# Kernel optimization log

Measured on AMD Instinct MI355X. Metric: run time of the kernel, lower is better.

## Reference

```python
import jax, jax.numpy as jnp
from jax import lax
import numpy as np

B, C, H, W, HID = 16, 8, 512, 512, 16


def setup_inputs() -> dict:
    key = jax.random.key(0)
    k1, k2, k3, k4, k5 = jax.random.split(key, 5)
    x = jax.random.normal(k1, (B, C, H, W), dtype=jnp.float32)
    w1_w = jax.random.normal(k2, (HID, 4 * C), dtype=jnp.float32) * 0.1  # 1x1 conv 32->16
    w1_b = jax.random.normal(k3, (HID,), dtype=jnp.float32) * 0.1
    w2_w = jax.random.normal(k4, (C, HID), dtype=jnp.float32) * 0.1     # 1x1 conv 16->8, no bias
    update_mask = jax.random.randint(k5, (B, 1, H, W), 0, 2, dtype=jnp.int32)  # floor(rand+0.5)
    return {"x": x, "w1_w": w1_w, "w1_b": w1_b, "w2_w": w2_w, "update_mask": update_mask}


def _fixed_filters(dtype):
    ident = jnp.zeros((3, 3), dtype).at[1, 1].set(1.0)
    sobel_x = jnp.array([[-1.0, 0.0, 1.0], [-2.0, 0.0, 2.0], [-1.0, 0.0, 1.0]], dtype) / 8.0
    lap = jnp.array([[1.0, 2.0, 1.0], [2.0, -12.0, 2.0], [1.0, 2.0, 1.0]], dtype) / 16.0
    return jnp.stack([ident, sobel_x, sobel_x.T, lap])  # [4,3,3]


def _perception(x):
    b, c, h, w = x.shape
    filt = _fixed_filters(x.dtype)
    xp = jnp.pad(x, ((0, 0), (0, 0), (1, 1), (1, 1)), mode="wrap")  # circular pad
    y = lax.conv_general_dilated(
        xp.reshape(b * c, 1, h + 2, w + 2), filt[:, None], (1, 1), "VALID",
        dimension_numbers=("NCHW", "OIHW", "NCHW"))  # [b*c,4,h,w]
    return y.reshape(b, c * 4, h, w)  # channel-major: (c0f0..c0f3, c1f0.., ...)


def reference(x, w1_w, w1_b, w2_w, update_mask):
    dt = 1.0
    y = _perception(x)                                   # [B,4C,H,W]
    y = jax.nn.relu(jnp.einsum("bchw,oc->bohw", y, w1_w) + w1_b[None, :, None, None])
    y = jnp.einsum("bchw,oc->bohw", y, w2_w)             # [B,C,H,W]
    return x + dt * y * update_mask.astype(x.dtype)
```

## Files before the change

kernel.cpp:

```cpp
#include <hip/hip_runtime.h>
#include <stdint.h>


constexpr int B = 16, C = 8, H = 512, W = 512, HID = 16;
constexpr int HW = H * W;
constexpr int BUF = 3 * W;

#define PKFMA_S(acc, w, p) \
    asm("v_pk_fma_f32 %0, %1, %2, %0" : "+v"(acc) : "s"(w), "v"(p))
#define PKFMA_V(acc, a, b) \
    asm("v_pk_fma_f32 %0, %1, %2, %0" : "+v"(acc) : "v"(a), "v"(b))

typedef const __attribute__((address_space(1))) void* as1cp;
typedef __attribute__((address_space(3))) void* as3p;

__global__ void repack_weights(const float* __restrict__ w1w,
                               const float* __restrict__ w2w,
                               float2* __restrict__ wd) {
    const int i = blockIdx.x * 256 + threadIdx.x;
    if (i < 512) {
        const int c = i >> 6, r = i & 63, h = r >> 2, f = r & 3;
        const float v = w1w[h * 32 + c * 4 + f];
        wd[i] = make_float2(v, v);
    } else if (i < 640) {
        const float v = w2w[i - 512];
        wd[i] = make_float2(v, v);
    }
}

__global__ __launch_bounds__(256, 6) void nca_step_kernel(
    const float* __restrict__ x,
    const float* __restrict__ w1b,
    const int*   __restrict__ mask,
    float*       __restrict__ out,
    const float2* __restrict__ wd)
{
    __shared__ float S[2 * BUF];

    const int bid = blockIdx.x;
    const int l   = (bid & 7) * 1024 + (bid >> 3);
    const int b   = l >> 9;
    const int y   = l & (H - 1);

    const int tx   = threadIdx.x;
    const int x0   = tx << 1;
    const int lane = tx & 63;
    const int wv   = tx >> 6;

    const int ym = (y - 1) & (H - 1);
    const int yp = (y + 1) & (H - 1);
    const int xm1 = (x0 - 1) & (W - 1);
    const int xp2 = (x0 + 2) & (W - 1);

    const float* xb = x + (size_t)b * C * HW;
    const int pix = y * W + x0;

    const int hh = wv & 1;
    const int g1 = ((wv < 2) ? ym : y) * W + hh * 256 + lane * 4;
    const int l1 = ((wv < 2) ? 0 : W) + hh * 256;
    const int g2 = yp * W + hh * 256 + lane * 4;
    const int l2 = 2 * W + hh * 256;

#define STAGE(ch, bufo) do {                                               \
    const float* cb_ = xb + (ch) * HW;                                     \
    __builtin_amdgcn_global_load_lds((as1cp)(cb_ + g1),                    \
                                     (as3p)(S + (bufo) + l1), 16, 0, 0);   \
    if (wv < 2)                                                            \
        __builtin_amdgcn_global_load_lds((as1cp)(cb_ + g2),                \
                                         (as3p)(S + (bufo) + l2), 16, 0, 0); \
    } while (0)

#define COMPCH(ch, bufo) do {                                              \
    const float* R0 = S + (bufo);                                          \
    const float* R1 = R0 + W;                                              \
    const float* R2 = R1 + W;                                              \
    const float2 vm = *(const float2*)(R0 + x0);                           \
    const float2 vc = *(const float2*)(R1 + x0);                           \
    const float2 vp = *(const float2*)(R2 + x0);                           \
    const float cm[4] = {R0[xm1], vm.x, vm.y, R0[xp2]};                    \
    const float cc[4] = {R1[xm1], vc.x, vc.y, R1[xp2]};                    \
    const float cp[4] = {R2[xm1], vp.x, vp.y, R2[xp2]};                    \
    float s_[4], d_[4];                                                    \
    _Pragma("unroll") for (int i = 0; i < 4; ++i) {                        \
        s_[i] = fmaf(2.0f, cc[i], cm[i] + cp[i]);                          \
        d_[i] = cp[i] - cm[i]; }                                           \
    const float sx0  = (s_[2] - s_[0]) * 0.125f;                           \
    const float sx1  = (s_[3] - s_[1]) * 0.125f;                           \
    const float sy0  = fmaf(2.0f, d_[1], d_[0] + d_[2]) * 0.125f;          \
    const float sy1  = fmaf(2.0f, d_[2], d_[1] + d_[3]) * 0.125f;          \
    const float lap0 = fmaf(fmaf(2.0f, s_[1], s_[0] + s_[2]), 0.0625f, -cc[1]); \
    const float lap1 = fmaf(fmaf(2.0f, s_[2], s_[1] + s_[3]), 0.0625f, -cc[2]); \
    const float2 idn2 = make_float2(cc[1], cc[2]);                         \
    const float2 sx2  = make_float2(sx0, sx1);                             \
    const float2 sy2  = make_float2(sy0, sy1);                             \
    const float2 lp2  = make_float2(lap0, lap1);                           \
    const float2* wch = wd + (ch) * 64;                                    \
    _Pragma("unroll") for (int h = 0; h < HID; ++h) {                      \
        PKFMA_S(acc[h], wch[h * 4 + 0], idn2);                             \
        PKFMA_S(acc[h], wch[h * 4 + 1], sx2);                              \
        PKFMA_S(acc[h], wch[h * 4 + 2], sy2);                              \
        PKFMA_S(acc[h], wch[h * 4 + 3], lp2); } } while (0)

    const int2 m2 = *(const int2*)(mask + (size_t)b * HW + pix);

    float2 acc[HID];
#pragma unroll
    for (int h = 0; h < HID; ++h) {
        const float bv = w1b[h];
        acc[h] = make_float2(bv, bv);
    }

    STAGE(0, 0);
    __syncthreads();
    STAGE(1, BUF); COMPCH(0, 0);   __syncthreads();
    STAGE(2, 0);   COMPCH(1, BUF); __syncthreads();
    STAGE(3, BUF); COMPCH(2, 0);   __syncthreads();
    STAGE(4, 0);   COMPCH(3, BUF); __syncthreads();
    STAGE(5, BUF); COMPCH(4, 0);   __syncthreads();
    STAGE(6, 0);   COMPCH(5, BUF); __syncthreads();
    STAGE(7, BUF); COMPCH(6, 0);   __syncthreads();
                   COMPCH(7, BUF);

#undef STAGE
#undef COMPCH

#pragma unroll
    for (int h = 0; h < HID; ++h) {
        acc[h].x = fmaxf(acc[h].x, 0.0f);
        acc[h].y = fmaxf(acc[h].y, 0.0f);
    }

    const float2 mf = make_float2((float)m2.x, (float)m2.y);
    const float2* w2d = wd + 512;
    float* ob = out + (size_t)b * C * HW;

    float2 xo = *(const float2*)(xb + pix);
#pragma unroll
    for (int o = 0; o < C; ++o) {
        float2 xn;
        if (o + 1 < C) xn = *(const float2*)(xb + (o + 1) * HW + pix);
        float2 v = make_float2(0.0f, 0.0f);
#pragma unroll
        for (int h = 0; h < HID; ++h)
            PKFMA_S(v, w2d[o * 16 + h], acc[h]);
        PKFMA_V(xo, v, mf);
        *(float2*)(ob + o * HW + pix) = xo;
        xo = xn;
    }
}

extern "C" void kernel_launch(void* const* d_in, const int* in_sizes, int n_in,
                              void* d_out, int out_size, void* d_ws, size_t ws_size,
                              hipStream_t stream) {
    const float* x    = (const float*)d_in[0];
    const float* w1w  = (const float*)d_in[1];
    const float* w1b  = (const float*)d_in[2];
    const float* w2w  = (const float*)d_in[3];
    const int*   mask = (const int*)d_in[4];
    float* out = (float*)d_out;
    float2* wd = (float2*)d_ws;

    hipLaunchKernelGGL(repack_weights, dim3(3), dim3(256), 0, stream,
                       w1w, w2w, wd);
    hipLaunchKernelGGL(nca_step_kernel, dim3(B * H), dim3(256), 0, stream,
                       x, w1b, mask, out, wd);
}
```

Measured before the change: 96.07 us.

## Triple-buffer LDS staging with vmcnt waits and balanced per-wave row loads

Replaces the double-buffered channel staging with a three-deep LDS ring. Two channels are now in flight, and each stage waits only for its own loads via s_waitcnt vmcnt(2) before a raw s_barrier, instead of a full __syncthreads. Row loading is rebalanced so every wave issues two async global-to-LDS loads per stage. The fourth wave uses its slots to stage the mask row into LDS, and the mask is then read from LDS rather than with a separate global load. The aim is to hide global latency better in this memory-bound stencil. The cost is doubled LDS per block, which may limit occupancy, and the mask row being re-fetched redundantly on every stage.

```diff
diff --git a/kernel.cpp b/kernel.cpp
--- a/kernel.cpp
+++ b/kernel.cpp
@@ -4,12 +4,17 @@
 
 constexpr int B = 16, C = 8, H = 512, W = 512, HID = 16;
 constexpr int HW = H * W;
-constexpr int BUF = 3 * W;
+constexpr int BUF = 3 * W + 512;
 
 #define PKFMA_S(acc, w, p) \
     asm("v_pk_fma_f32 %0, %1, %2, %0" : "+v"(acc) : "s"(w), "v"(p))
 #define PKFMA_V(acc, a, b) \
     asm("v_pk_fma_f32 %0, %1, %2, %0" : "+v"(acc) : "v"(a), "v"(b))
+
+#define VMWAIT2 asm volatile("s_waitcnt vmcnt(2)" ::: "memory")
+#define VMWAIT0 asm volatile("s_waitcnt vmcnt(0)" ::: "memory")
+#define BARRIER do { __builtin_amdgcn_s_barrier(); \
+                     __builtin_amdgcn_sched_barrier(0); } while (0)
 
 typedef const __attribute__((address_space(1))) void* as1cp;
 typedef __attribute__((address_space(3))) void* as3p;
@@ -35,7 +40,7 @@
     float*       __restrict__ out,
     const float2* __restrict__ wd)
 {
-    __shared__ float S[2 * BUF];
+    __shared__ float S[3 * BUF];
 
     const int bid = blockIdx.x;
     const int l   = (bid & 7) * 1024 + (bid >> 3);
@@ -55,20 +60,24 @@
     const float* xb = x + (size_t)b * C * HW;
     const int pix = y * W + x0;
 
-    const int hh = wv & 1;
-    const int g1 = ((wv < 2) ? ym : y) * W + hh * 256 + lane * 4;
-    const int l1 = ((wv < 2) ? 0 : W) + hh * 256;
-    const int g2 = yp * W + hh * 256 + lane * 4;
-    const int l2 = 2 * W + hh * 256;
+    int r1f, l1, r2f, l2;
+    if (wv == 0)      { r1f = ym * W;       l1 = 0;       r2f = y * W;        l2 = W; }
+    else if (wv == 1) { r1f = ym * W + 256; l1 = 256;     r2f = y * W + 256;  l2 = W + 256; }
+    else if (wv == 2) { r1f = yp * W;       l1 = 2 * W;   r2f = yp * W + 256; l2 = 2 * W + 256; }
+    else              { r1f = 0;            l1 = 3 * W;   r2f = 256;          l2 = 3 * W + 256; }
+    const float* sb = (wv == 3) ? (const float*)(mask + (size_t)b * HW + (size_t)y * W)
+                                : xb;
+    const int sm = (wv == 3) ? 0 : HW;
+    const int g1 = r1f + lane * 4;
+    const int g2 = r2f + lane * 4;
 
 #define STAGE(ch, bufo) do {                                               \
-    const float* cb_ = xb + (ch) * HW;                                     \
-    __builtin_amdgcn_global_load_lds((as1cp)(cb_ + g1),                    \
-                                     (as3p)(S + (bufo) + l1), 16, 0, 0);   \
-    if (wv < 2)                                                            \
-        __builtin_amdgcn_global_load_lds((as1cp)(cb_ + g2),                \
-                                         (as3p)(S + (bufo) + l2), 16, 0, 0); \
-    } while (0)
+    const float* s1_ = sb + (ch) * sm + g1;                                \
+    const float* s2_ = sb + (ch) * sm + g2;                                \
+    __builtin_amdgcn_global_load_lds((as1cp)s1_, (as3p)(S + (bufo) + l1),  \
+                                     16, 0, 0);                            \
+    __builtin_amdgcn_global_load_lds((as1cp)s2_, (as3p)(S + (bufo) + l2),  \
+                                     16, 0, 0); } while (0)
 
 #define COMPCH(ch, bufo) do {                                              \
     const float* R0 = S + (bufo);                                          \
@@ -101,7 +110,8 @@
         PKFMA_S(acc[h], wch[h * 4 + 2], sy2);                              \
         PKFMA_S(acc[h], wch[h * 4 + 3], lp2); } } while (0)
 
-    const int2 m2 = *(const int2*)(mask + (size_t)b * HW + pix);
+    STAGE(0, 0);
+    STAGE(1, BUF);
 
     float2 acc[HID];
 #pragma unroll
@@ -110,16 +120,14 @@
         acc[h] = make_float2(bv, bv);
     }
 
-    STAGE(0, 0);
-    __syncthreads();
-    STAGE(1, BUF); COMPCH(0, 0);   __syncthreads();
-    STAGE(2, 0);   COMPCH(1, BUF); __syncthreads();
-    STAGE(3, BUF); COMPCH(2, 0);   __syncthreads();
-    STAGE(4, 0);   COMPCH(3, BUF); __syncthreads();
-    STAGE(5, BUF); COMPCH(4, 0);   __syncthreads();
-    STAGE(6, 0);   COMPCH(5, BUF); __syncthreads();
-    STAGE(7, BUF); COMPCH(6, 0);   __syncthreads();
-                   COMPCH(7, BUF);
+    VMWAIT2; BARRIER; STAGE(2, 2 * BUF); COMPCH(0, 0);
+    VMWAIT2; BARRIER; STAGE(3, 0);       COMPCH(1, BUF);
+    VMWAIT2; BARRIER; STAGE(4, BUF);     COMPCH(2, 2 * BUF);
+    VMWAIT2; BARRIER; STAGE(5, 2 * BUF); COMPCH(3, 0);
+    VMWAIT2; BARRIER; STAGE(6, 0);       COMPCH(4, BUF);
+    VMWAIT2; BARRIER; STAGE(7, BUF);     COMPCH(5, 2 * BUF);
+    VMWAIT2; BARRIER;                    COMPCH(6, 0);
+    VMWAIT0; BARRIER;                    COMPCH(7, BUF);
 
 #undef STAGE
 #undef COMPCH
@@ -130,7 +138,10 @@
         acc[h].y = fmaxf(acc[h].y, 0.0f);
     }
 
+    const int* mlds = (const int*)(S + BUF + 3 * W);
+    const int2 m2 = *(const int2*)(mlds + x0);
     const float2 mf = make_float2((float)m2.x, (float)m2.y);
+
     const float2* w2d = wd + 512;
     float* ob = out + (size_t)b * C * HW;
 
```

Result: slower. 103.4 us (+7.7%).

## Stage two channels per barrier and reuse LDS center values for residual

Applied to the files above, without the earlier changes.

The LDS pipeline now stages two channels per step with a larger double buffer, halving the number of barriers from eight to four phases. Each wave issues three async global-to-LDS loads per stage. The center-row values read from LDS are kept in registers and reused for the residual add, so the epilogue no longer re-reads x from global memory. This uses twice the LDS per block and holds 16 more registers live, which may lower occupancy.

```diff
diff --git a/kernel.cpp b/kernel.cpp
--- a/kernel.cpp
+++ b/kernel.cpp
@@ -4,7 +4,7 @@
 
 constexpr int B = 16, C = 8, H = 512, W = 512, HID = 16;
 constexpr int HW = H * W;
-constexpr int BUF = 3 * W;
+constexpr int BUF2 = 2 * 3 * W;
 
 #define PKFMA_S(acc, w, p) \
     asm("v_pk_fma_f32 %0, %1, %2, %0" : "+v"(acc) : "s"(w), "v"(p))
@@ -35,7 +35,7 @@
     float*       __restrict__ out,
     const float2* __restrict__ wd)
 {
-    __shared__ float S[2 * BUF];
+    __shared__ float S[2 * BUF2];
 
     const int bid = blockIdx.x;
     const int l   = (bid & 7) * 1024 + (bid >> 3);
@@ -55,28 +55,31 @@
     const float* xb = x + (size_t)b * C * HW;
     const int pix = y * W + x0;
 
-    const int hh = wv & 1;
-    const int g1 = ((wv < 2) ? ym : y) * W + hh * 256 + lane * 4;
-    const int l1 = ((wv < 2) ? 0 : W) + hh * 256;
-    const int g2 = yp * W + hh * 256 + lane * 4;
-    const int l2 = 2 * W + hh * 256;
+    const int2 m2 = *(const int2*)(mask + (size_t)b * HW + pix);
 
-#define STAGE(ch, bufo) do {                                               \
-    const float* cb_ = xb + (ch) * HW;                                     \
-    __builtin_amdgcn_global_load_lds((as1cp)(cb_ + g1),                    \
-                                     (as3p)(S + (bufo) + l1), 16, 0, 0);   \
-    if (wv < 2)                                                            \
-        __builtin_amdgcn_global_load_lds((as1cp)(cb_ + g2),                \
-                                         (as3p)(S + (bufo) + l2), 16, 0, 0); \
-    } while (0)
+    const int k0 = wv * 3;
 
-#define COMPCH(ch, bufo) do {                                              \
-    const float* R0 = S + (bufo);                                          \
+#define STAGE2(cb, bufo) do {                                              \
+    _Pragma("unroll") for (int j = 0; j < 3; ++j) {                        \
+        const int k  = k0 + j;                                             \
+        const int ch = k / 6, rr = (k % 6) >> 1, hf = k & 1;               \
+        const int grow = (rr == 0) ? ym : ((rr == 1) ? y : yp);            \
+        const float* src = xb + ((cb) + ch) * HW + grow * W + hf * 256     \
+                              + lane * 4;                                  \
+        __builtin_amdgcn_global_load_lds(                                  \
+            (as1cp)src,                                                    \
+            (as3p)(S + (bufo) + ch * 1536 + rr * 512 + hf * 256),          \
+            16, 0, 0);                                                     \
+    } } while (0)
+
+#define COMPCH(ch, bufo, cc_) do {                                         \
+    const float* R0 = S + (bufo) + (cc_) * 1536;                           \
     const float* R1 = R0 + W;                                              \
     const float* R2 = R1 + W;                                              \
     const float2 vm = *(const float2*)(R0 + x0);                           \
     const float2 vc = *(const float2*)(R1 + x0);                           \
     const float2 vp = *(const float2*)(R2 + x0);                           \
+    xs##ch = vc;                       \
     const float cm[4] = {R0[xm1], vm.x, vm.y, R0[xp2]};                    \
     const float cc[4] = {R1[xm1], vc.x, vc.y, R1[xp2]};                    \
     const float cp[4] = {R2[xm1], vp.x, vp.y, R2[xp2]};                    \
@@ -101,8 +104,6 @@
         PKFMA_S(acc[h], wch[h * 4 + 2], sy2);                              \
         PKFMA_S(acc[h], wch[h * 4 + 3], lp2); } } while (0)
 
-    const int2 m2 = *(const int2*)(mask + (size_t)b * HW + pix);
-
     float2 acc[HID];
 #pragma unroll
     for (int h = 0; h < HID; ++h) {
@@ -110,18 +111,19 @@
         acc[h] = make_float2(bv, bv);
     }
 
-    STAGE(0, 0);
+    float2 xs0, xs1, xs2, xs3, xs4, xs5, xs6, xs7;
+
+    STAGE2(0, 0);
     __syncthreads();
-    STAGE(1, BUF); COMPCH(0, 0);   __syncthreads();
-    STAGE(2, 0);   COMPCH(1, BUF); __syncthreads();
-    STAGE(3, BUF); COMPCH(2, 0);   __syncthreads();
-    STAGE(4, 0);   COMPCH(3, BUF); __syncthreads();
-    STAGE(5, BUF); COMPCH(4, 0);   __syncthreads();
-    STAGE(6, 0);   COMPCH(5, BUF); __syncthreads();
-    STAGE(7, BUF); COMPCH(6, 0);   __syncthreads();
-                   COMPCH(7, BUF);
+    STAGE2(2, BUF2); COMPCH(0, 0, 0);    COMPCH(1, 0, 1);
+    __syncthreads();
+    STAGE2(4, 0);    COMPCH(2, BUF2, 0); COMPCH(3, BUF2, 1);
+    __syncthreads();
+    STAGE2(6, BUF2); COMPCH(4, 0, 0);    COMPCH(5, 0, 1);
+    __syncthreads();
+                     COMPCH(6, BUF2, 0); COMPCH(7, BUF2, 1);
 
-#undef STAGE
+#undef STAGE2
 #undef COMPCH
 
 #pragma unroll
@@ -134,19 +136,17 @@
     const float2* w2d = wd + 512;
     float* ob = out + (size_t)b * C * HW;
 
-    float2 xo = *(const float2*)(xb + pix);
-#pragma unroll
-    for (int o = 0; o < C; ++o) {
-        float2 xn;
-        if (o + 1 < C) xn = *(const float2*)(xb + (o + 1) * HW + pix);
-        float2 v = make_float2(0.0f, 0.0f);
-#pragma unroll
-        for (int h = 0; h < HID; ++h)
-            PKFMA_S(v, w2d[o * 16 + h], acc[h]);
-        PKFMA_V(xo, v, mf);
-        *(float2*)(ob + o * HW + pix) = xo;
-        xo = xn;
-    }
+#define EPI(o, xsv) do {                                                   \
+    float2 v = make_float2(0.0f, 0.0f);                                    \
+    _Pragma("unroll") for (int h = 0; h < HID; ++h)                        \
+        PKFMA_S(v, w2d[(o) * 16 + h], acc[h]);                             \
+    float2 r = xsv;                                                        \
+    PKFMA_V(r, v, mf);                           \
+    *(float2*)(ob + (o) * HW + pix) = r; } while (0)
+
+    EPI(0, xs0); EPI(1, xs1); EPI(2, xs2); EPI(3, xs3);
+    EPI(4, xs4); EPI(5, xs5); EPI(6, xs6); EPI(7, xs7);
+#undef EPI
 }
 
 extern "C" void kernel_launch(void* const* d_in, const int* in_sizes, int n_in,
```

New measurement: 101.9 us. 6.1% more time.

## Process two rows per block and stage two channels per step; fold filter scales into weights

Applied to the files above, without the earlier changes.

Each 512-thread block now computes two adjacent output rows, so the 4 staged input rows per channel serve two rows and halo reloads drop from 3 to 2 rows per output row. Two channels are staged per pipeline step, which halves the number of barriers. The sobel and laplacian scale factors and the identity-minus-center term are folded into the repacked weights, removing per-pixel multiplies. The cost is more LDS per block (16 KB→32 KB) and larger blocks, which may limit occupancy.

```diff
diff --git a/kernel.cpp b/kernel.cpp
--- a/kernel.cpp
+++ b/kernel.cpp
@@ -3,8 +3,9 @@
 
 
 constexpr int B = 16, C = 8, H = 512, W = 512, HID = 16;
-constexpr int HW = H * W;
-constexpr int BUF = 3 * W;
+constexpr int HW  = H * W;
+constexpr int CHF = 4 * W;
+constexpr int BUF = 2 * CHF;
 
 #define PKFMA_S(acc, w, p) \
     asm("v_pk_fma_f32 %0, %1, %2, %0" : "+v"(acc) : "s"(w), "v"(p))
@@ -20,7 +21,11 @@
     const int i = blockIdx.x * 256 + threadIdx.x;
     if (i < 512) {
         const int c = i >> 6, r = i & 63, h = r >> 2, f = r & 3;
-        const float v = w1w[h * 32 + c * 4 + f];
+        const float* wr = w1w + h * 32 + c * 4;
+        float v;
+        if (f == 0)      v = wr[0] - wr[3];
+        else if (f == 3) v = wr[3] * 0.0625f;
+        else             v = wr[f] * 0.125f;
         wd[i] = make_float2(v, v);
     } else if (i < 640) {
         const float v = w2w[i - 512];
@@ -28,7 +33,7 @@
     }
 }
 
-__global__ __launch_bounds__(256, 6) void nca_step_kernel(
+__global__ __launch_bounds__(512, 8) void nca_step_kernel(
     const float* __restrict__ x,
     const float* __restrict__ w1b,
     const int*   __restrict__ mask,
@@ -38,40 +43,46 @@
     __shared__ float S[2 * BUF];
 
     const int bid = blockIdx.x;
-    const int l   = (bid & 7) * 1024 + (bid >> 3);
-    const int b   = l >> 9;
-    const int y   = l & (H - 1);
+    const int l   = (bid & 7) * 512 + (bid >> 3);
+    const int b   = l >> 8;
+    const int pr  = l & 255;
+    const int y0  = pr << 1;
+    const int y1  = y0 + 1;
 
-    const int tx   = threadIdx.x;
+    const int tid  = threadIdx.x;
+    const int rel  = tid >> 8;
+    const int tx   = tid & 255;
     const int x0   = tx << 1;
-    const int lane = tx & 63;
-    const int wv   = tx >> 6;
+    const int lane = tid & 63;
+    const int wv   = tid >> 6;
 
-    const int ym = (y - 1) & (H - 1);
-    const int yp = (y + 1) & (H - 1);
+    const int ym  = (y0 - 1) & (H - 1);
+    const int yp2 = (y1 + 1) & (H - 1);
     const int xm1 = (x0 - 1) & (W - 1);
     const int xp2 = (x0 + 2) & (W - 1);
 
     const float* xb = x + (size_t)b * C * HW;
+    const int y   = y0 + rel;
     const int pix = y * W + x0;
 
-    const int hh = wv & 1;
-    const int g1 = ((wv < 2) ? ym : y) * W + hh * 256 + lane * 4;
-    const int l1 = ((wv < 2) ? 0 : W) + hh * 256;
-    const int g2 = yp * W + hh * 256 + lane * 4;
-    const int l2 = 2 * W + hh * 256;
+    const int2 m2 = *(const int2*)(mask + (size_t)b * HW + pix);
+    const float2 mf = make_float2((float)m2.x, (float)m2.y);
 
-#define STAGE(ch, bufo) do {                                               \
-    const float* cb_ = xb + (ch) * HW;                                     \
-    __builtin_amdgcn_global_load_lds((as1cp)(cb_ + g1),                    \
-                                     (as3p)(S + (bufo) + l1), 16, 0, 0);   \
-    if (wv < 2)                                                            \
-        __builtin_amdgcn_global_load_lds((as1cp)(cb_ + g2),                \
-                                         (as3p)(S + (bufo) + l2), 16, 0, 0); \
-    } while (0)
+    const int ch_l = wv >> 2;
+    const int rr   = wv & 3;
+    const int grow = (rr == 0) ? ym : ((rr == 1) ? y0 : ((rr == 2) ? y1 : yp2));
+    const int goff = grow * W + lane * 4;
+    const int loff = ch_l * CHF + rr * W;
 
-#define COMPCH(ch, bufo) do {                                              \
-    const float* R0 = S + (bufo);                                          \
+#define STAGE(cb, bufo) do {                                               \
+    const float* s_ = xb + ((cb) + ch_l) * HW + goff;                      \
+    float* d_ = S + (bufo) + loff;                                         \
+    __builtin_amdgcn_global_load_lds((as1cp)s_, (as3p)d_, 16, 0, 0);       \
+    __builtin_amdgcn_global_load_lds((as1cp)(s_ + 256), (as3p)(d_ + 256),  \
+                                     16, 0, 0); } while (0)
+
+#define COMPCH(ch, cl, bufo) do {                                          \
+    const float* R0 = S + (bufo) + (cl) * CHF + rel * W;                   \
     const float* R1 = R0 + W;                                              \
     const float* R2 = R1 + W;                                              \
     const float2 vm = *(const float2*)(R0 + x0);                           \
@@ -84,24 +95,19 @@
     _Pragma("unroll") for (int i = 0; i < 4; ++i) {                        \
         s_[i] = fmaf(2.0f, cc[i], cm[i] + cp[i]);                          \
         d_[i] = cp[i] - cm[i]; }                                           \
-    const float sx0  = (s_[2] - s_[0]) * 0.125f;                           \
-    const float sx1  = (s_[3] - s_[1]) * 0.125f;                           \
-    const float sy0  = fmaf(2.0f, d_[1], d_[0] + d_[2]) * 0.125f;          \
-    const float sy1  = fmaf(2.0f, d_[2], d_[1] + d_[3]) * 0.125f;          \
-    const float lap0 = fmaf(fmaf(2.0f, s_[1], s_[0] + s_[2]), 0.0625f, -cc[1]); \
-    const float lap1 = fmaf(fmaf(2.0f, s_[2], s_[1] + s_[3]), 0.0625f, -cc[2]); \
+               \
     const float2 idn2 = make_float2(cc[1], cc[2]);                         \
-    const float2 sx2  = make_float2(sx0, sx1);                             \
-    const float2 sy2  = make_float2(sy0, sy1);                             \
-    const float2 lp2  = make_float2(lap0, lap1);                           \
+    const float2 sx2  = make_float2(s_[2] - s_[0], s_[3] - s_[1]);         \
+    const float2 sy2  = make_float2(fmaf(2.0f, d_[1], d_[0] + d_[2]),      \
+                                    fmaf(2.0f, d_[2], d_[1] + d_[3]));     \
+    const float2 lp2  = make_float2(fmaf(2.0f, s_[1], s_[0] + s_[2]),      \
+                                    fmaf(2.0f, s_[2], s_[1] + s_[3]));     \
     const float2* wch = wd + (ch) * 64;                                    \
     _Pragma("unroll") for (int h = 0; h < HID; ++h) {                      \
         PKFMA_S(acc[h], wch[h * 4 + 0], idn2);                             \
         PKFMA_S(acc[h], wch[h * 4 + 1], sx2);                              \
         PKFMA_S(acc[h], wch[h * 4 + 2], sy2);                              \
         PKFMA_S(acc[h], wch[h * 4 + 3], lp2); } } while (0)
-
-    const int2 m2 = *(const int2*)(mask + (size_t)b * HW + pix);
 
     float2 acc[HID];
 #pragma unroll
@@ -112,14 +118,10 @@
 
     STAGE(0, 0);
     __syncthreads();
-    STAGE(1, BUF); COMPCH(0, 0);   __syncthreads();
-    STAGE(2, 0);   COMPCH(1, BUF); __syncthreads();
-    STAGE(3, BUF); COMPCH(2, 0);   __syncthreads();
-    STAGE(4, 0);   COMPCH(3, BUF); __syncthreads();
-    STAGE(5, BUF); COMPCH(4, 0);   __syncthreads();
-    STAGE(6, 0);   COMPCH(5, BUF); __syncthreads();
-    STAGE(7, BUF); COMPCH(6, 0);   __syncthreads();
-                   COMPCH(7, BUF);
+    STAGE(2, BUF); COMPCH(0, 0, 0);   COMPCH(1, 1, 0);   __syncthreads();
+    STAGE(4, 0);   COMPCH(2, 0, BUF); COMPCH(3, 1, BUF); __syncthreads();
+    STAGE(6, BUF); COMPCH(4, 0, 0);   COMPCH(5, 1, 0);   __syncthreads();
+                   COMPCH(6, 0, BUF); COMPCH(7, 1, BUF);
 
 #undef STAGE
 #undef COMPCH
@@ -130,7 +132,6 @@
         acc[h].y = fmaxf(acc[h].y, 0.0f);
     }
 
-    const float2 mf = make_float2((float)m2.x, (float)m2.y);
     const float2* w2d = wd + 512;
     float* ob = out + (size_t)b * C * HW;
 
@@ -162,6 +163,6 @@
 
     hipLaunchKernelGGL(repack_weights, dim3(3), dim3(256), 0, stream,
                        w1w, w2w, wd);
-    hipLaunchKernelGGL(nca_step_kernel, dim3(B * H), dim3(256), 0, stream,
+    hipLaunchKernelGGL(nca_step_kernel, dim3(B * H / 2), dim3(512), 0, stream,
                        x, w1b, mask, out, wd);
 }
```

Measured after the change: 96.99 us. No clear change (+1.0%).
